# Kernel optimization log

Measured on AMD Instinct MI355X. Metric: run time of the kernel, lower is better.

## Reference

```python
import jax, jax.numpy as jnp
import numpy as np
from jax import lax

G = 16            # graphs in batch
N0 = 2048         # total nodes (128 per graph)
IN_CH = 64
HID = 128
KS = (103, 83)    # ceil(0.8*128), ceil(0.8*103): per-graph nodes kept by each ASAPooling
NEG_SLOPE = 0.2   # ASAPooling leaky_relu slope


def _masked_col_max(M, x, chunk=4):
    # out[i, c] = max_{j : M[j, i]} x[j, c]  (scatter-max over incoming edges), feature-chunked
    N, C = x.shape
    xr = x.T.reshape(C // chunk, chunk, N)
    @jax.checkpoint
    def f(xc):  # [chunk, N_j]
        v = jnp.where(M[None, :, :], xc[:, :, None], -1e30)  # [chunk, j, i]
        return v.max(axis=1)
    return lax.map(f, xr).reshape(C, N).T


def _graph_conv(x, A, w_rel, b_rel, w_root):
    # PyG GraphConv(aggr='mean'): lin_rel(mean_j w_ji * x_j) + lin_root(x); A[src,dst]
    deg = jnp.maximum((A != 0).sum(0).astype(x.dtype), 1.0)  # incoming edge count
    agg = (A.T @ x) / deg[:, None]
    return agg @ w_rel.T + b_rel + x @ w_root.T


def _gpool(x):  # global_mean_pool over equal-sized contiguous graphs
    return x.reshape(G, -1, x.shape[-1]).mean(axis=1)


def _asap_pool(x, A, k, lin_w, lin_b, att_w, att_b, le1_w, le1_b, le2_w, le3_w, le3_b):
    N, C = x.shape
    one = jnp.asarray(1.0, x.dtype)
    A = jnp.where(jnp.eye(N, dtype=bool), one, A)  # add_remaining_self_loops(fill=1)
    M = A != 0
    Mf = M.astype(x.dtype)
    # master query: max over incoming neighbors, then Linear
    q = _masked_col_max(M, x) @ lin_w.T + lin_b                     # [N, C]
    a_q, a_x = att_w[:C], att_w[C:]                                 # att(cat([x_q_i, x_j]))
    logits = jax.nn.leaky_relu((x @ a_x)[:, None] + (q @ a_q)[None, :] + att_b, NEG_SLOPE)  # [j, i]
    S = jnp.where(M, jax.nn.softmax(jnp.where(M, logits, -1e30), axis=0), 0.0)
    x_new = S.T @ x                                                  # cluster reps
    # fitness = sigmoid(LEConv(x_new)): lin3(x_i) + sum_j (lin1(x_j) - lin2(x_i)) over edges
    deg = Mf.sum(0)
    a = x_new @ le1_w + le1_b
    b = x_new @ le2_w
    fitness = jax.nn.sigmoid(Mf.T @ a - deg * b + x_new @ le3_w + le3_b)  # [N]
    n_cur = N // G
    idx = lax.top_k(fitness.reshape(G, n_cur), k)[1]                 # per-graph top-k
    perm = (idx + jnp.arange(G)[:, None] * n_cur).reshape(-1)        # [G*k], grouped by graph
    x_out = x_new[perm] * fitness[perm][:, None]
    S_sel = S[:, perm]                                               # [N, K]
    A2 = S_sel.T @ (A @ S_sel)                                       # S^T A S coarsening
    A2 = jnp.where(jnp.eye(G * k, dtype=bool), one, A2)              # fill_diag(1)
    return x_out, A2


def _forward(x, edge_index, c0_wrel, c0_brel, c0_wroot, cw_rel, cb_rel, cw_root,
             p_lin_w, p_lin_b, p_att_w, p_att_b, p_le1_w, p_le1_b, p_le2_w,
             p_le3_w, p_le3_b, lin1_w, lin1_b, lin2_w, lin2_b):
    A = jnp.zeros((N0, N0), x.dtype).at[edge_index[0], edge_index[1]].add(1.0)
    h = jax.nn.relu(_graph_conv(x, A, c0_wrel, c0_brel, c0_wroot))
    xs = [_gpool(h)]
    p = 0
    for i in range(4):  # num_layers - 1 convs
        h = jax.nn.relu(_graph_conv(h, A, cw_rel[i], cb_rel[i], cw_root[i]))
        xs.append(_gpool(h))
        if i % 2 == 0 and i < 3:
            h, A = _asap_pool(h, A, KS[p], p_lin_w[p], p_lin_b[p], p_att_w[p], p_att_b[p],
                              p_le1_w[p], p_le1_b[p], p_le2_w[p], p_le3_w[p], p_le3_b[p])
            p += 1
    j = jnp.concatenate(xs, axis=-1)                                  # JK 'cat': [G, 5*HID]
    z = jax.nn.relu(j @ lin1_w.T + lin1_b)                            # dropout: eval mode (identity)
    z = z @ lin2_w.T + lin2_b
    return jax.nn.log_softmax(z, axis=-1)


def setup_inputs() -> dict:
    key = jax.random.key(0)
    rng = np.random.default_rng(0)
    n, deg = N0 // G, 16
    sc = rng.random((G, n, n))
    sc[:, np.arange(n), np.arange(n)] = -1.0  # no self loops
    dst = np.argsort(-sc, axis=-1)[:, :, :deg]  # 16 distinct neighbors per node
    src = np.broadcast_to(np.arange(n)[None, :, None], dst.shape)
    off = (np.arange(G) * n)[:, None, None]
    edge_index = jnp.asarray(np.stack([(src + off).ravel(), (dst + off).ravel()]), dtype=jnp.int32)
    ks = jax.random.split(key, 16)
    def lin(k, shape, fan_in):
        return jax.random.normal(k, shape, jnp.float32) / np.sqrt(fan_in)
    return dict(
        x=jax.random.normal(ks[0], (N0, IN_CH), jnp.float32),
        edge_index=edge_index,
        c0_wrel=lin(ks[1], (HID, IN_CH), IN_CH),
        c0_brel=jnp.zeros((HID,), jnp.float32),
        c0_wroot=lin(ks[2], (HID, IN_CH), IN_CH),
        cw_rel=lin(ks[3], (4, HID, HID), HID),
        cb_rel=jnp.zeros((4, HID), jnp.float32),
        cw_root=lin(ks[4], (4, HID, HID), HID),
        p_lin_w=lin(ks[5], (2, HID, HID), HID),
        p_lin_b=jnp.zeros((2, HID), jnp.float32),
        p_att_w=lin(ks[6], (2, 2 * HID), 2 * HID),
        p_att_b=jnp.zeros((2,), jnp.float32),
        p_le1_w=lin(ks[7], (2, HID), HID),
        p_le1_b=jnp.zeros((2,), jnp.float32),
        p_le2_w=lin(ks[8], (2, HID), HID),
        p_le3_w=lin(ks[9], (2, HID), HID),
        p_le3_b=jnp.zeros((2,), jnp.float32),
        lin1_w=lin(ks[10], (HID, 5 * HID), 5 * HID),
        lin1_b=jnp.zeros((HID,), jnp.float32),
        lin2_w=lin(ks[11], (2, HID), HID),
        lin2_b=jnp.zeros((2,), jnp.float32),
    )


def reference(x, edge_index, c0_wrel, c0_brel, c0_wroot, cw_rel, cb_rel, cw_root,
              p_lin_w, p_lin_b, p_att_w, p_att_b, p_le1_w, p_le1_b, p_le2_w,
              p_le3_w, p_le3_b, lin1_w, lin1_b, lin2_w, lin2_b):
    return _forward(x, edge_index, c0_wrel, c0_brel, c0_wroot, cw_rel, cb_rel, cw_root,
                    p_lin_w, p_lin_b, p_att_w, p_att_b, p_le1_w, p_le1_b, p_le2_w,
                    p_le3_w, p_le3_b, lin1_w, lin1_b, lin2_w, lin2_b)
```

## Files before the change

### kernel.cpp

```cpp
#include <hip/hip_runtime.h>

#define NEG_SLOPE 0.2f
typedef unsigned int u32;

__global__ __launch_bounds__(256) void k_build(const int* __restrict__ ei,
                                               u32* __restrict__ Mb,
                                               u32* __restrict__ Rb, int E)
{
    int e = blockIdx.x * 256 + threadIdx.x;
    if (e >= E) return;
    int s = ei[e], d = ei[E + e];
    int g = s >> 7, ls = s & 127, ld = d & 127;
    atomicOr(&Mb[(g * 128 + ld) * 4 + (ls >> 5)], 1u << (ls & 31));
    atomicOr(&Rb[(g * 128 + ls) * 4 + (ld >> 5)], 1u << (ld & 31));
}

__global__ __launch_bounds__(128) void k_prep(
    const float* __restrict__ lin_w, const float* __restrict__ lin_b,
    const float* __restrict__ att_w,
    float* __restrict__ v_out, float* __restrict__ c0_out)
{
    const int p = blockIdx.x;
    const float* lw = lin_w + p * 16384;
    const float* lb = lin_b + p * 128;
    const float* aw = att_w + p * 256;
    const int c = threadIdx.x;
    float s = 0.f;
    for (int c2 = 0; c2 < 128; ++c2) s += aw[c2] * lw[c2 * 128 + c];
    v_out[p * 128 + c] = s;
    if (c < 64) {
        float s0 = aw[c] * lb[c] + aw[c + 64] * lb[c + 64];
        for (int off = 32; off; off >>= 1) s0 += __shfl_xor(s0, off);
        if (c == 0) c0_out[p] = s0;
    }
}

__global__ __launch_bounds__(512) void k_agg_mask(
    const float* __restrict__ h, const u32* __restrict__ Mb,
    float* __restrict__ agg, int n, int Cin)
{
    const int g = blockIdx.x;
    const int q4 = Cin >> 2;
    int idx = blockIdx.y * 512 + threadIdx.x;
    if (idx >= n * q4) return;
    int j = idx / q4, c4 = (idx - j * q4) << 2;
    const u32* m = Mb + (g * 128 + j) * 4;
    u32 m0 = m[0], m1 = m[1], m2 = m[2], m3 = m[3];
    float dv = fmaxf((float)(__popc(m0) + __popc(m1) + __popc(m2) + __popc(m3)), 1.0f);
    const float* hg = h + (size_t)g * n * Cin + c4;
    float sx = 0.f, sy = 0.f, sz = 0.f, sw = 0.f;
    u32 wds[4] = { m0, m1, m2, m3 };
    #pragma unroll
    for (int ww = 0; ww < 4; ++ww) {
        u32 u = wds[ww];
        while (u) {
            int i = (ww << 5) + __ffs(u) - 1; u &= u - 1u;
            float4 hv = *(const float4*)(hg + (size_t)i * Cin);
            sx += hv.x; sy += hv.y; sz += hv.z; sw += hv.w;
        }
    }
    float4 o; o.x = sx / dv; o.y = sy / dv; o.z = sz / dv; o.w = sw / dv;
    *(float4*)(agg + ((size_t)g * n + j) * Cin + c4) = o;
}

__global__ __launch_bounds__(512) void k_agg_dense(
    const float* __restrict__ h, const float* __restrict__ AT,
    const u32* __restrict__ Mb, float* __restrict__ agg, int n)
{
    const int C = 128;
    const int g = blockIdx.x;
    int idx = blockIdx.y * 512 + threadIdx.x;
    if (idx >= n * 32) return;
    int j = idx >> 5, c4 = (idx & 31) << 2;
    const u32* m = Mb + (g * 128 + j) * 4;
    float dv = fmaxf((float)(__popc(m[0]) + __popc(m[1]) + __popc(m[2]) + __popc(m[3])), 1.0f);
    const float* Aj = AT + ((size_t)g * n + j) * n;
    const float* hg = h + (size_t)g * n * C + c4;
    float sx = 0.f, sy = 0.f, sz = 0.f, sw = 0.f;
    for (int i = 0; i < n; ++i) {
        float a = Aj[i];
        float4 hv = *(const float4*)(hg + (size_t)i * C);
        sx += a * hv.x; sy += a * hv.y; sz += a * hv.z; sw += a * hv.w;
    }
    float4 o; o.x = sx / dv; o.y = sy / dv; o.z = sz / dv; o.w = sw / dv;
    *(float4*)(agg + ((size_t)g * n + j) * C + c4) = o;
}

__global__ __launch_bounds__(256) void k_out(
    const float* __restrict__ h, const float* __restrict__ agg,
    const float* __restrict__ wrel, const float* __restrict__ brel,
    const float* __restrict__ wroot,
    float* __restrict__ h_out, float* __restrict__ xs,
    int n, int Cin)
{
    const int g = blockIdx.x;
    const int jb = blockIdx.y * 32;
    const int tid = threadIdx.x;
    const int tx = tid & 31, ty = tid >> 5;
    __shared__ float Xs[32][34];
    __shared__ float Ws[128][34];
    float acc[4][4] = {};
    const int K = 2 * Cin;
    const float* hg = h + (size_t)g * n * Cin;
    const float* ag = agg + (size_t)g * n * Cin;

    for (int kk = 0; kk < K; kk += 32) {
        const float* Xsrc = (kk < Cin) ? (ag + kk) : (hg + kk - Cin);
        #pragma unroll
        for (int it = 0; it < 2; ++it) {
            int l = it * 256 + tid;
            int kp = l & 15, j = l >> 4;
            int jg = jb + j; if (jg > n - 1) jg = n - 1;
            float2 v = *(const float2*)(Xsrc + (size_t)jg * Cin + kp * 2);
            *(float2*)&Xs[j][kp * 2] = v;
        }
        const float* Wsrc = (kk < Cin) ? (wrel + kk) : (wroot + kk - Cin);
        #pragma unroll
        for (int it = 0; it < 8; ++it) {
            int l = it * 256 + tid;
            int kp = l & 15, c2 = l >> 4;
            float2 v = *(const float2*)(Wsrc + (size_t)c2 * Cin + kp * 2);
            *(float2*)&Ws[c2][kp * 2] = v;
        }
        __syncthreads();
        #pragma unroll
        for (int kp = 0; kp < 16; ++kp) {
            float2 xv[4], wv[4];
            #pragma unroll
            for (int r = 0; r < 4; ++r) xv[r] = *(const float2*)&Xs[ty * 4 + r][kp * 2];
            #pragma unroll
            for (int q = 0; q < 4; ++q) wv[q] = *(const float2*)&Ws[tx + 32 * q][kp * 2];
            #pragma unroll
            for (int r = 0; r < 4; ++r)
                #pragma unroll
                for (int q = 0; q < 4; ++q)
                    acc[r][q] += xv[r].x * wv[q].x + xv[r].y * wv[q].y;
        }
        __syncthreads();
    }

    float ps[4] = { 0.f, 0.f, 0.f, 0.f };
    #pragma unroll
    for (int q = 0; q < 4; ++q) {
        int c2 = tx + 32 * q;
        float b = brel[c2];
        #pragma unroll
        for (int r = 0; r < 4; ++r) {
            int jg = jb + ty * 4 + r;
            if (jg < n) {
                float v = fmaxf(acc[r][q] + b, 0.0f);
                h_out[((size_t)g * n + jg) * 128 + c2] = v;
                ps[q] += v;
            }
        }
    }
    float* red = &Ws[0][0];
    #pragma unroll
    for (int q = 0; q < 4; ++q) red[ty * 128 + tx + 32 * q] = ps[q];
    __syncthreads();
    if (tid < 128) {
        float s = 0.f;
        #pragma unroll
        for (int t = 0; t < 8; ++t) s += red[t * 128 + tid];
        atomicAdd(&xs[g * 128 + tid], s / (float)n);
    }
}

__global__ __launch_bounds__(512) void k_attn(
    const float* __restrict__ h, const u32* __restrict__ Mb_g,
    const float* __restrict__ v_g, const float* __restrict__ c0_g,
    const float* __restrict__ att_w,
    float* __restrict__ qa_g, float* __restrict__ xa_g, int n)
{
    const int g = blockIdx.x;
    const int tid = threadIdx.x;
    const int hw = tid >> 5, ln = tid & 31;
    const float* hg = h + (size_t)g * n * 128;
    const int j = blockIdx.y * 16 + hw;
    if (j < n) {
        u32 m[4];
        m[0] = Mb_g[(g * 128 + j) * 4 + 0]; m[1] = Mb_g[(g * 128 + j) * 4 + 1];
        m[2] = Mb_g[(g * 128 + j) * 4 + 2]; m[3] = Mb_g[(g * 128 + j) * 4 + 3];
        m[j >> 5] |= 1u << (j & 31);
        float4 mx = make_float4(-1e30f, -1e30f, -1e30f, -1e30f);
        #pragma unroll
        for (int ww = 0; ww < 4; ++ww) {
            u32 u = m[ww];
            while (u) {
                int i = (ww << 5) + __ffs(u) - 1; u &= u - 1u;
                float4 hv = *(const float4*)(hg + (size_t)i * 128 + ln * 4);
                mx.x = fmaxf(mx.x, hv.x); mx.y = fmaxf(mx.y, hv.y);
                mx.z = fmaxf(mx.z, hv.z); mx.w = fmaxf(mx.w, hv.w);
            }
        }
        float4 vv = *(const float4*)(v_g + ln * 4);
        float acc = mx.x * vv.x + mx.y * vv.y + mx.z * vv.z + mx.w * vv.w;
        #pragma unroll
        for (int off = 16; off; off >>= 1) acc += __shfl_xor(acc, off, 32);
        if (ln == 0) qa_g[g * 128 + j] = acc + c0_g[0];
    }
    const int i = blockIdx.y * 16 + hw;
    if (i < n) {
        float4 hv = *(const float4*)(hg + (size_t)i * 128 + ln * 4);
        float4 aw = *(const float4*)(att_w + 128 + ln * 4);
        float s = hv.x * aw.x + hv.y * aw.y + hv.z * aw.z + hv.w * aw.w;
        #pragma unroll
        for (int off = 16; off; off >>= 1) s += __shfl_xor(s, off, 32);
        if (ln == 0) xa_g[g * 128 + i] = s;
    }
}

__global__ __launch_bounds__(512) void k_soft(
    const u32* __restrict__ Mb_g, const float* __restrict__ qa_g,
    const float* __restrict__ xa_g, const float* __restrict__ att_bp,
    float* __restrict__ S_cm, int n)
{
    const int g = blockIdx.x;
    const int tid = threadIdx.x, lane = tid & 63, wid = tid >> 6;
    const int j = blockIdx.y * 8 + wid;
    if (j >= n) return;
    const float att_b = att_bp[0];
    u32 m[4];
    m[0] = Mb_g[(g * 128 + j) * 4 + 0]; m[1] = Mb_g[(g * 128 + j) * 4 + 1];
    m[2] = Mb_g[(g * 128 + j) * 4 + 2]; m[3] = Mb_g[(g * 128 + j) * 4 + 3];
    m[j >> 5] |= 1u << (j & 31);
    const float qaj = qa_g[g * 128 + j];
    const int i0 = lane, i1 = lane + 64;
    const bool b0 = (i0 < n) && ((m[i0 >> 5] >> (i0 & 31)) & 1u);
    const bool b1 = (i1 < n) && ((m[i1 >> 5] >> (i1 & 31)) & 1u);
    float l0 = -1e30f, l1 = -1e30f;
    if (b0) { float t = xa_g[g * 128 + i0] + qaj + att_b; l0 = (t >= 0.f) ? t : NEG_SLOPE * t; }
    if (b1) { float t = xa_g[g * 128 + i1] + qaj + att_b; l1 = (t >= 0.f) ? t : NEG_SLOPE * t; }
    float mm = fmaxf(l0, l1);
    for (int off = 32; off; off >>= 1) mm = fmaxf(mm, __shfl_xor(mm, off));
    float e0 = b0 ? expf(l0 - mm) : 0.f;
    float e1 = b1 ? expf(l1 - mm) : 0.f;
    float s = e0 + e1;
    for (int off = 32; off; off >>= 1) s += __shfl_xor(s, off);
    float* Sj = S_cm + ((size_t)g * 128 + j) * 128;
    if (i0 < n) Sj[i0] = e0 / s;
    if (i1 < n) Sj[i1] = e1 / s;
}

__global__ __launch_bounds__(512) void k_xnew(
    const float* __restrict__ S_cm, const float* __restrict__ h,
    float* __restrict__ xn, int n)
{
    const int g = blockIdx.x;
    int idx = blockIdx.y * 512 + threadIdx.x;
    if (idx >= n * 32) return;
    int j = idx >> 5, c4 = (idx & 31) << 2;
    const float* Sj = S_cm + ((size_t)g * 128 + j) * 128;
    const float* hg = h + (size_t)g * n * 128 + c4;
    float sx = 0.f, sy = 0.f, sz = 0.f, sw = 0.f;
    for (int i = 0; i < n; ++i) {
        float sv = Sj[i];
        float4 hv = *(const float4*)(hg + (size_t)i * 128);
        sx += sv * hv.x; sy += sv * hv.y; sz += sv * hv.z; sw += sv * hv.w;
    }
    float4 o; o.x = sx; o.y = sy; o.z = sz; o.w = sw;
    *(float4*)(xn + ((size_t)g * 128 + j) * 128 + c4) = o;
}

__global__ __launch_bounds__(512) void k_fit(
    const float* __restrict__ xn, const u32* __restrict__ Mb_g,
    const float* __restrict__ S_cm,
    const float* __restrict__ le1_w, const float* __restrict__ le1_bp,
    const float* __restrict__ le2_w, const float* __restrict__ le3_w,
    const float* __restrict__ le3_bp,
    float* __restrict__ h_out, float* __restrict__ Sselr, float* __restrict__ SselrT,
    int n, int k, int kpad)
{
    const int g = blockIdx.x;
    const float* xg = xn + (size_t)g * 128 * 128;
    __shared__ float a_s[128], b_s[128], c3_s[128], fit_s[128];
    __shared__ int perm_s[128];
    const int tid = threadIdx.x, lane = tid & 63, wid = tid >> 6;

    for (int j = wid; j < n; j += 8) {
        float x0 = xg[j * 128 + lane], x1 = xg[j * 128 + 64 + lane];
        float s1 = x0 * le1_w[lane] + x1 * le1_w[64 + lane];
        float s2 = x0 * le2_w[lane] + x1 * le2_w[64 + lane];
        float s3 = x0 * le3_w[lane] + x1 * le3_w[64 + lane];
        for (int off = 32; off; off >>= 1) {
            s1 += __shfl_xor(s1, off);
            s2 += __shfl_xor(s2, off);
            s3 += __shfl_xor(s3, off);
        }
        if (lane == 0) { a_s[j] = s1 + le1_bp[0]; b_s[j] = s2; c3_s[j] = s3; }
    }
    __syncthreads();
    for (int j = tid; j < n; j += 512) {
        u32 m[4];
        m[0] = Mb_g[(g * 128 + j) * 4 + 0]; m[1] = Mb_g[(g * 128 + j) * 4 + 1];
        m[2] = Mb_g[(g * 128 + j) * 4 + 2]; m[3] = Mb_g[(g * 128 + j) * 4 + 3];
        m[j >> 5] |= 1u << (j & 31);
        float dv = (float)(__popc(m[0]) + __popc(m[1]) + __popc(m[2]) + __popc(m[3]));
        float s = 0.f;
        #pragma unroll
        for (int ww = 0; ww < 4; ++ww) {
            u32 u = m[ww];
            while (u) { int i = (ww << 5) + __ffs(u) - 1; u &= u - 1u; s += a_s[i]; }
        }
        float f = s - dv * b_s[j] + c3_s[j] + le3_bp[0];
        fit_s[j] = 1.0f / (1.0f + expf(-f));
    }
    __syncthreads();
    for (int j = tid; j < n; j += 512) {
        float fj = fit_s[j];
        int r = 0;
        for (int j2 = 0; j2 < n; ++j2) {
            float f2 = fit_s[j2];
            if (f2 > fj || (f2 == fj && j2 < j)) ++r;
        }
        if (r < k) perm_s[r] = j;
    }
    __syncthreads();
    for (int idx = tid; idx < k * 32; idx += 512) {
        int r = idx >> 5, c4 = (idx & 31) << 2;
        int p = perm_s[r]; float f = fit_s[p];
        float4 v = *(const float4*)(xg + p * 128 + c4);
        v.x *= f; v.y *= f; v.z *= f; v.w *= f;
        *(float4*)(h_out + ((size_t)g * k + r) * 128 + c4) = v;
    }
    for (int idx = tid; idx < k * 32; idx += 512) {
        int r = idx >> 5, c4 = (idx & 31) << 2;
        float4 v = *(const float4*)(S_cm + ((size_t)g * 128 + perm_s[r]) * 128 + c4);
        *(float4*)(SselrT + ((size_t)g * 128 + r) * 128 + c4) = v;
    }
    for (int idx = tid; idx < k * n; idx += 512) {
        int cc = idx / n, i = idx - cc * n;
        Sselr[((size_t)g * 128 + i) * kpad + cc] =
            S_cm[((size_t)g * 128 + perm_s[cc]) * 128 + i];
    }
}

__global__ __launch_bounds__(512) void k_T_mask(
    const u32* __restrict__ Rb, const float* __restrict__ Sselr,
    float* __restrict__ T, int n, int k, int kpad)
{
    const int g = blockIdx.x;
    const int ccq = (k + 3) >> 2;
    int idx = blockIdx.y * 512 + threadIdx.x;
    if (idx >= n * ccq) return;
    int i = idx / ccq, c4 = (idx - i * ccq) << 2;
    u32 m[4];
    m[0] = Rb[(g * 128 + i) * 4 + 0]; m[1] = Rb[(g * 128 + i) * 4 + 1];
    m[2] = Rb[(g * 128 + i) * 4 + 2]; m[3] = Rb[(g * 128 + i) * 4 + 3];
    m[i >> 5] |= 1u << (i & 31);
    float sx = 0.f, sy = 0.f, sz = 0.f, sw = 0.f;
    #pragma unroll
    for (int ww = 0; ww < 4; ++ww) {
        u32 u = m[ww];
        while (u) {
            int j = (ww << 5) + __ffs(u) - 1; u &= u - 1u;
            float4 v = *(const float4*)(Sselr + ((size_t)g * 128 + j) * kpad + c4);
            sx += v.x; sy += v.y; sz += v.z; sw += v.w;
        }
    }
    float4 o; o.x = sx; o.y = sy; o.z = sz; o.w = sw;
    *(float4*)(T + ((size_t)g * 128 + i) * kpad + c4) = o;
}

__global__ __launch_bounds__(512) void k_T_dense(
    const float* __restrict__ A, const float* __restrict__ Sselr,
    float* __restrict__ T, int n, int k, int kpad)
{
    const int g = blockIdx.x;
    const int ccq = (k + 3) >> 2;
    int idx = blockIdx.y * 512 + threadIdx.x;
    if (idx >= n * ccq) return;
    int i = idx / ccq, c4 = (idx - i * ccq) << 2;
    const float* Ai = A + ((size_t)g * n + i) * n;
    float sx = 0.f, sy = 0.f, sz = 0.f, sw = 0.f;
    for (int j = 0; j < n; ++j) {
        float a = Ai[j];
        float4 v = *(const float4*)(Sselr + ((size_t)g * 128 + j) * kpad + c4);
        sx += a * v.x; sy += a * v.y; sz += a * v.z; sw += a * v.w;
    }
    float4 o; o.x = sx; o.y = sy; o.z = sz; o.w = sw;
    *(float4*)(T + ((size_t)g * 128 + i) * kpad + c4) = o;
}

__global__ __launch_bounds__(512) void k_A2(
    const float* __restrict__ SselrT, const float* __restrict__ T,
    float* __restrict__ A_out, float* __restrict__ AT_out,
    u32* __restrict__ Mb_out, int n, int k, int kpad)
{
    const int g = blockIdx.x;
    int idx = blockIdx.y * 512 + threadIdx.x;
    if (idx >= k * k) return;
    int r = idx / k, cc = idx - r * k;
    const float* Sr = SselrT + ((size_t)g * 128 + r) * 128;
    const float* Tg = T + (size_t)g * 128 * kpad;
    float s = 0.f;
    for (int i = 0; i < n; ++i) s += Sr[i] * Tg[i * kpad + cc];
    float val = (r == cc) ? 1.0f : s;
    A_out[((size_t)g * k + r) * k + cc] = val;
    AT_out[((size_t)g * k + cc) * k + r] = val;
    if (val != 0.0f)
        atomicOr(&Mb_out[((size_t)g * 128 + cc) * 4 + (r >> 5)], 1u << (r & 31));
}

__global__ __launch_bounds__(256) void k_final(
    const float* __restrict__ xs,
    const float* __restrict__ w1, const float* __restrict__ b1,
    const float* __restrict__ w2, const float* __restrict__ b2,
    float* __restrict__ out)
{
    const int g = blockIdx.x;
    __shared__ float j_s[640];
    __shared__ float z1[128];
    const int tid = threadIdx.x, lane = tid & 63, wid = tid >> 6;

    for (int idx = tid; idx < 640; idx += 256) {
        int t = idx >> 7, c = idx & 127;
        j_s[idx] = xs[t * 2048 + g * 128 + c];
    }
    __syncthreads();
    for (int c2 = wid; c2 < 128; c2 += 4) {
        const float* wrow = w1 + (size_t)c2 * 640;
        float s = 0.f;
        #pragma unroll
        for (int it = 0; it < 10; ++it) {
            int kk = it * 64 + lane;
            s += j_s[kk] * wrow[kk];
        }
        for (int off = 32; off; off >>= 1) s += __shfl_xor(s, off);
        if (lane == 0) z1[c2] = fmaxf(s + b1[c2], 0.0f);
    }
    __syncthreads();
    if (wid == 0) {
        float zv0 = z1[lane], zv1 = z1[lane + 64];
        float za = zv0 * w2[lane] + zv1 * w2[lane + 64];
        float zb = zv0 * w2[128 + lane] + zv1 * w2[192 + lane];
        for (int off = 32; off; off >>= 1) {
            za += __shfl_xor(za, off);
            zb += __shfl_xor(zb, off);
        }
        if (lane == 0) {
            za += b2[0]; zb += b2[1];
            float m = fmaxf(za, zb);
            float lse = m + logf(expf(za - m) + expf(zb - m));
            out[g * 2 + 0] = za - lse;
            out[g * 2 + 1] = zb - lse;
        }
    }
}

extern "C" void kernel_launch(void* const* d_in, const int* in_sizes, int n_in,
                              void* d_out, int out_size, void* d_ws, size_t ws_size,
                              hipStream_t stream)
{
    (void)n_in; (void)out_size; (void)ws_size;
    const float* x        = (const float*)d_in[0];
    const int*   ei       = (const int*)  d_in[1];
    const float* c0_wrel  = (const float*)d_in[2];
    const float* c0_brel  = (const float*)d_in[3];
    const float* c0_wroot = (const float*)d_in[4];
    const float* cw_rel   = (const float*)d_in[5];
    const float* cb_rel   = (const float*)d_in[6];
    const float* cw_root  = (const float*)d_in[7];
    const float* p_lin_w  = (const float*)d_in[8];
    const float* p_lin_b  = (const float*)d_in[9];
    const float* p_att_w  = (const float*)d_in[10];
    const float* p_att_b  = (const float*)d_in[11];
    const float* p_le1_w  = (const float*)d_in[12];
    const float* p_le1_b  = (const float*)d_in[13];
    const float* p_le2_w  = (const float*)d_in[14];
    const float* p_le3_w  = (const float*)d_in[15];
    const float* p_le3_b  = (const float*)d_in[16];
    const float* lin1_w   = (const float*)d_in[17];
    const float* lin1_b   = (const float*)d_in[18];
    const float* lin2_w   = (const float*)d_in[19];
    const float* lin2_b   = (const float*)d_in[20];
    float* out = (float*)d_out;

    const int E = in_sizes[1] / 2;

    u32*   Mb1 = (u32*)d_ws;
    u32*   Rb1 = Mb1 + 8192;
    float* xsf = (float*)(Rb1 + 8192);
    u32*   Mb2 = (u32*)(xsf + 10240);
    u32*   Mb3 = Mb2 + 8192;
    float* qaw = (float*)(Mb3 + 8192);
    float* xaw = qaw + 2048;
    float* vbuf = xaw + 2048;
    float* c0buf = vbuf + 256;
    float* agg = c0buf + 4;
    float* hA  = agg + 262144;
    float* hB  = hA  + 262144;
    float* Scm = hB  + 262144;
    float* xnw = Scm + 262144;
    float* Ssr = xnw + 262144;
    float* SsT = Ssr + 229376;
    float* A2  = SsT + 262144;
    float* A2T = A2  + 169744;
    float* A3  = A2T + 169744;
    float* A3T = A3  + 110224;
    float* Tw  = agg;

    hipMemsetAsync(d_ws, 0, (8192 + 8192 + 10240 + 8192 + 8192) * 4, stream);
    k_build<<<(E + 255) / 256, 256, 0, stream>>>(ei, Mb1, Rb1, E);
    k_prep<<<2, 128, 0, stream>>>(p_lin_w, p_lin_b, p_att_w, vbuf, c0buf);

    k_agg_mask<<<dim3(16, 4), 512, 0, stream>>>(x, Mb1, agg, 128, 64);
    k_out<<<dim3(16, 4), 256, 0, stream>>>(x, agg, c0_wrel, c0_brel, c0_wroot,
                                           hA, xsf + 0 * 2048, 128, 64);
    k_agg_mask<<<dim3(16, 8), 512, 0, stream>>>(hA, Mb1, agg, 128, 128);
    k_out<<<dim3(16, 4), 256, 0, stream>>>(hA, agg, cw_rel, cb_rel, cw_root,
                                           hB, xsf + 1 * 2048, 128, 128);
    k_attn<<<dim3(16, 8), 512, 0, stream>>>(hB, Mb1, vbuf, c0buf, p_att_w, qaw, xaw, 128);
    k_soft<<<dim3(16, 16), 512, 0, stream>>>(Mb1, qaw, xaw, p_att_b, Scm, 128);
    k_xnew<<<dim3(16, 8), 512, 0, stream>>>(Scm, hB, xnw, 128);
    k_fit<<<16, 512, 0, stream>>>(xnw, Mb1, Scm,
                                  p_le1_w, p_le1_b, p_le2_w, p_le3_w, p_le3_b,
                                  hA, Ssr, SsT, 128, 103, 112);
    k_T_mask<<<dim3(16, 7), 512, 0, stream>>>(Rb1, Ssr, Tw, 128, 103, 112);
    k_A2<<<dim3(16, 21), 512, 0, stream>>>(SsT, Tw, A2, A2T, Mb2, 128, 103, 112);
    k_agg_dense<<<dim3(16, 7), 512, 0, stream>>>(hA, A2T, Mb2, agg, 103);
    k_out<<<dim3(16, 4), 256, 0, stream>>>(hA, agg, cw_rel + 16384, cb_rel + 128,
                                           cw_root + 16384, hB, xsf + 2 * 2048, 103, 128);
    k_agg_dense<<<dim3(16, 7), 512, 0, stream>>>(hB, A2T, Mb2, agg, 103);
    k_out<<<dim3(16, 4), 256, 0, stream>>>(hB, agg, cw_rel + 2 * 16384, cb_rel + 2 * 128,
                                           cw_root + 2 * 16384, hA, xsf + 3 * 2048, 103, 128);
    k_attn<<<dim3(16, 7), 512, 0, stream>>>(hA, Mb2, vbuf + 128, c0buf + 1,
                                            p_att_w + 256, qaw, xaw, 103);
    k_soft<<<dim3(16, 13), 512, 0, stream>>>(Mb2, qaw, xaw, p_att_b + 1, Scm, 103);
    k_xnew<<<dim3(16, 7), 512, 0, stream>>>(Scm, hA, xnw, 103);
    k_fit<<<16, 512, 0, stream>>>(xnw, Mb2, Scm,
                                  p_le1_w + 128, p_le1_b + 1, p_le2_w + 128,
                                  p_le3_w + 128, p_le3_b + 1,
                                  hB, Ssr, SsT, 103, 83, 96);
    k_T_dense<<<dim3(16, 5), 512, 0, stream>>>(A2, Ssr, Tw, 103, 83, 96);
    k_A2<<<dim3(16, 14), 512, 0, stream>>>(SsT, Tw, A3, A3T, Mb3, 103, 83, 96);
    k_agg_dense<<<dim3(16, 6), 512, 0, stream>>>(hB, A3T, Mb3, agg, 83);
    k_out<<<dim3(16, 3), 256, 0, stream>>>(hB, agg, cw_rel + 3 * 16384, cb_rel + 3 * 128,
                                           cw_root + 3 * 16384, hA, xsf + 4 * 2048, 83, 128);

    k_final<<<16, 256, 0, stream>>>(xsf, lin1_w, lin1_b, lin2_w, lin2_b, out);
}
```

Baseline: 586.5 us.

## Rewrite GraphConv output GEMM as per-row lane-group dot products with shuffle reduction

Replaces the shared-memory tiled GEMM in k_out with a kernel where a group of CIN/2 lanes computes one node row, each lane holding a float4 slice of the concatenated [agg, h] input and reducing dot products across the group with xor shuffles. The grid gets many more blocks (8 rows per block for CIN=128), so there is more parallelism for these small layers. In exchange, weight reuse across rows is lost, every group rereads the full weight matrix, and each output needs a serial shuffle reduction with only one writing lane.

Measured after the change: 754.0 us. +28.6%, slower.

```diff
diff --git a/kernel.cpp b/kernel.cpp
--- a/kernel.cpp
+++ b/kernel.cpp
@@ -86,82 +86,55 @@
     *(float4*)(agg + ((size_t)g * n + j) * C + c4) = o;
 }
 
-__global__ __launch_bounds__(256) void k_out(
+template<int CIN>
+__global__ __launch_bounds__(512) void k_out(
     const float* __restrict__ h, const float* __restrict__ agg,
     const float* __restrict__ wrel, const float* __restrict__ brel,
     const float* __restrict__ wroot,
     float* __restrict__ h_out, float* __restrict__ xs,
-    int n, int Cin)
-{
-    const int g = blockIdx.x;
-    const int jb = blockIdx.y * 32;
+    int n)
+{
+    constexpr int L = CIN >> 1;
+    constexpr int G = 512 / L;
+    constexpr int HALF = L >> 1;
+    const int g = blockIdx.x;
+    const int gg = threadIdx.x / L;
+    const int l  = threadIdx.x % L;
+    const int jg = blockIdx.y * G + gg;
+    __shared__ float tile[G * 128];
+
+    if (jg < n) {
+        const float* xsrc = (l < HALF)
+            ? (agg + ((size_t)g * n + jg) * CIN + (l << 2))
+            : (h   + ((size_t)g * n + jg) * CIN + ((l - HALF) << 2));
+        const float4 xv = *(const float4*)xsrc;
+        const float* wbase = (l < HALF) ? (wrel + (l << 2))
+                                        : (wroot + ((l - HALF) << 2));
+        for (int c2 = 0; c2 < 128; ++c2) {
+            float4 wv = *(const float4*)(wbase + (size_t)c2 * CIN);
+            float acc = xv.x * wv.x + xv.y * wv.y + xv.z * wv.z + xv.w * wv.w;
+            #pragma unroll
+            for (int off = L >> 1; off; off >>= 1)
+                acc += __shfl_xor(acc, off, L);
+            if (l == 0) tile[gg * 128 + c2] = fmaxf(acc + brel[c2], 0.0f);
+        }
+    } else {
+        for (int c2 = l; c2 < 128; c2 += L) tile[gg * 128 + c2] = 0.0f;
+    }
+    __syncthreads();
+
     const int tid = threadIdx.x;
-    const int tx = tid & 31, ty = tid >> 5;
-    __shared__ float Xs[32][34];
-    __shared__ float Ws[128][34];
-    float acc[4][4] = {};
-    const int K = 2 * Cin;
-    const float* hg = h + (size_t)g * n * Cin;
-    const float* ag = agg + (size_t)g * n * Cin;
-
-    for (int kk = 0; kk < K; kk += 32) {
-        const float* Xsrc = (kk < Cin) ? (ag + kk) : (hg + kk - Cin);
-        #pragma unroll
-        for (int it = 0; it < 2; ++it) {
-            int l = it * 256 + tid;
-            int kp = l & 15, j = l >> 4;
-            int jg = jb + j; if (jg > n - 1) jg = n - 1;
-            float2 v = *(const float2*)(Xsrc + (size_t)jg * Cin + kp * 2);
-            *(float2*)&Xs[j][kp * 2] = v;
-        }
-        const float* Wsrc = (kk < Cin) ? (wrel + kk) : (wroot + kk - Cin);
-        #pragma unroll
-        for (int it = 0; it < 8; ++it) {
-            int l = it * 256 + tid;
-            int kp = l & 15, c2 = l >> 4;
-            float2 v = *(const float2*)(Wsrc + (size_t)c2 * Cin + kp * 2);
-            *(float2*)&Ws[c2][kp * 2] = v;
-        }
-        __syncthreads();
-        #pragma unroll
-        for (int kp = 0; kp < 16; ++kp) {
-            float2 xv[4], wv[4];
-            #pragma unroll
-            for (int r = 0; r < 4; ++r) xv[r] = *(const float2*)&Xs[ty * 4 + r][kp * 2];
-            #pragma unroll
-            for (int q = 0; q < 4; ++q) wv[q] = *(const float2*)&Ws[tx + 32 * q][kp * 2];
-            #pragma unroll
-            for (int r = 0; r < 4; ++r)
-                #pragma unroll
-                for (int q = 0; q < 4; ++q)
-                    acc[r][q] += xv[r].x * wv[q].x + xv[r].y * wv[q].y;
-        }
-        __syncthreads();
-    }
-
-    float ps[4] = { 0.f, 0.f, 0.f, 0.f };
-    #pragma unroll
-    for (int q = 0; q < 4; ++q) {
-        int c2 = tx + 32 * q;
-        float b = brel[c2];
-        #pragma unroll
-        for (int r = 0; r < 4; ++r) {
-            int jg = jb + ty * 4 + r;
-            if (jg < n) {
-                float v = fmaxf(acc[r][q] + b, 0.0f);
-                h_out[((size_t)g * n + jg) * 128 + c2] = v;
-                ps[q] += v;
-            }
-        }
-    }
-    float* red = &Ws[0][0];
-    #pragma unroll
-    for (int q = 0; q < 4; ++q) red[ty * 128 + tx + 32 * q] = ps[q];
-    __syncthreads();
+    for (int idx = tid; idx < G * 32; idx += 512) {
+        int r = idx >> 5, c4 = (idx & 31) << 2;
+        int j2 = blockIdx.y * G + r;
+        if (j2 < n)
+            *(float4*)(h_out + ((size_t)g * n + j2) * 128 + c4) =
+                *(const float4*)(tile + r * 128 + c4);
+    }
     if (tid < 128) {
         float s = 0.f;
         #pragma unroll
-        for (int t = 0; t < 8; ++t) s += red[t * 128 + tid];
+        for (int r = 0; r < G; ++r) s += tile[r * 128 + tid];
         atomicAdd(&xs[g * 128 + tid], s / (float)n);
     }
 }
@@ -505,11 +478,11 @@
     k_prep<<<2, 128, 0, stream>>>(p_lin_w, p_lin_b, p_att_w, vbuf, c0buf);
 
     k_agg_mask<<<dim3(16, 4), 512, 0, stream>>>(x, Mb1, agg, 128, 64);
-    k_out<<<dim3(16, 4), 256, 0, stream>>>(x, agg, c0_wrel, c0_brel, c0_wroot,
-                                           hA, xsf + 0 * 2048, 128, 64);
+    k_out<64><<<dim3(16, 8), 512, 0, stream>>>(x, agg, c0_wrel, c0_brel, c0_wroot,
+                                               hA, xsf + 0 * 2048, 128);
     k_agg_mask<<<dim3(16, 8), 512, 0, stream>>>(hA, Mb1, agg, 128, 128);
-    k_out<<<dim3(16, 4), 256, 0, stream>>>(hA, agg, cw_rel, cb_rel, cw_root,
-                                           hB, xsf + 1 * 2048, 128, 128);
+    k_out<128><<<dim3(16, 16), 512, 0, stream>>>(hA, agg, cw_rel, cb_rel, cw_root,
+                                                 hB, xsf + 1 * 2048, 128);
     k_attn<<<dim3(16, 8), 512, 0, stream>>>(hB, Mb1, vbuf, c0buf, p_att_w, qaw, xaw, 128);
     k_soft<<<dim3(16, 16), 512, 0, stream>>>(Mb1, qaw, xaw, p_att_b, Scm, 128);
     k_xnew<<<dim3(16, 8), 512, 0, stream>>>(Scm, hB, xnw, 128);
@@ -519,11 +492,11 @@
     k_T_mask<<<dim3(16, 7), 512, 0, stream>>>(Rb1, Ssr, Tw, 128, 103, 112);
     k_A2<<<dim3(16, 21), 512, 0, stream>>>(SsT, Tw, A2, A2T, Mb2, 128, 103, 112);
     k_agg_dense<<<dim3(16, 7), 512, 0, stream>>>(hA, A2T, Mb2, agg, 103);
-    k_out<<<dim3(16, 4), 256, 0, stream>>>(hA, agg, cw_rel + 16384, cb_rel + 128,
-                                           cw_root + 16384, hB, xsf + 2 * 2048, 103, 128);
+    k_out<128><<<dim3(16, 13), 512, 0, stream>>>(hA, agg, cw_rel + 16384, cb_rel + 128,
+                                                 cw_root + 16384, hB, xsf + 2 * 2048, 103);
     k_agg_dense<<<dim3(16, 7), 512, 0, stream>>>(hB, A2T, Mb2, agg, 103);
-    k_out<<<dim3(16, 4), 256, 0, stream>>>(hB, agg, cw_rel + 2 * 16384, cb_rel + 2 * 128,
-                                           cw_root + 2 * 16384, hA, xsf + 3 * 2048, 103, 128);
+    k_out<128><<<dim3(16, 13), 512, 0, stream>>>(hB, agg, cw_rel + 2 * 16384, cb_rel + 2 * 128,
+                                                 cw_root + 2 * 16384, hA, xsf + 3 * 2048, 103);
     k_attn<<<dim3(16, 7), 512, 0, stream>>>(hA, Mb2, vbuf + 128, c0buf + 1,
                                             p_att_w + 256, qaw, xaw, 103);
     k_soft<<<dim3(16, 13), 512, 0, stream>>>(Mb2, qaw, xaw, p_att_b + 1, Scm, 103);
@@ -535,8 +508,8 @@
     k_T_dense<<<dim3(16, 5), 512, 0, stream>>>(A2, Ssr, Tw, 103, 83, 96);
     k_A2<<<dim3(16, 14), 512, 0, stream>>>(SsT, Tw, A3, A3T, Mb3, 103, 83, 96);
     k_agg_dense<<<dim3(16, 6), 512, 0, stream>>>(hB, A3T, Mb3, agg, 83);
-    k_out<<<dim3(16, 3), 256, 0, stream>>>(hB, agg, cw_rel + 3 * 16384, cb_rel + 3 * 128,
-                                           cw_root + 3 * 16384, hA, xsf + 4 * 2048, 83, 128);
+    k_out<128><<<dim3(16, 11), 512, 0, stream>>>(hB, agg, cw_rel + 3 * 16384, cb_rel + 3 * 128,
+                                                 cw_root + 3 * 16384, hA, xsf + 4 * 2048, 83);
 
     k_final<<<16, 256, 0, stream>>>(xsf, lin1_w, lin1_b, lin2_w, lin2_b, out);
 }
```
